# Optimization experiments

Measured on AMD Instinct MI355X. Metric: run time of the kernel, lower is better.

Reference implementation:

```python
import jax, jax.numpy as jnp
import numpy as np

EPS = 1e-05


def _nearest_upsample(x, H, W):
    # torch F.interpolate default mode='nearest': src_idx = floor(dst_idx * in/out)
    h, w = x.shape[-2], x.shape[-1]
    rows = (jnp.arange(H) * h) // H
    cols = (jnp.arange(W) * w) // W
    return x[..., rows[:, None], cols[None, :]]


def _dilate(mask, k):
    # Grayscale dilation with a flat (all-ones) k x k structuring element ==
    # k x k max filter (kornia dilation w/ ones kernel). Geodesic border: pad -inf
    p = (k - 1) // 2
    return jax.lax.reduce_window(
        mask, -jnp.inf, jax.lax.max,
        window_dimensions=(1, 1, k, k),
        window_strides=(1, 1, 1, 1),
        padding=[(0, 0), (0, 0), (p, k - 1 - p), (p, k - 1 - p)],
    )


def setup_inputs() -> dict:
    key = jax.random.key(0)
    k1, k2 = jax.random.split(key)
    small = jax.random.normal(k1, (2, 4, 1, 270, 480), dtype=jnp.float32)
    large = jax.random.uniform(k2, (2, 4, 1, 1080, 1920), dtype=jnp.float32)
    return {"small": small, "large": large, "dilate_width": 7, "sigmoid": 1}


def reference(small, large, dilate_width, sigmoid):
    B, T = small.shape[0], small.shape[1]
    s = small.reshape((B * T,) + small.shape[2:])   # [BT, C, h, w]
    l = large.reshape((B * T,) + large.shape[2:])   # [BT, C, H, W]
    H, W = l.shape[-2], l.shape[-1]
    up = _nearest_upsample(s, H, W)
    t = jax.nn.sigmoid(up) if sigmoid else up
    trans = ((t > EPS) & (t < 1.0 - EPS)).astype(l.dtype)
    if dilate_width >= 1:
        trans = _dilate(trans, dilate_width)
    out = trans * l + (1.0 - trans) * up
    return out.reshape(large.shape)
```

## Files before the change

kernel.cpp:

```cpp
#include <hip/hip_runtime.h>
#include <cmath>

#define HS 270
#define WS 480
#define HL 1080
#define WL 1920

typedef float f4 __attribute__((ext_vector_type(4)));

__global__ __launch_bounds__(256) void PRM_77824807403842_kernel(
    const float* __restrict__ sml,
    const float* __restrict__ lrg,
    const int* __restrict__ sigp,
    float* __restrict__ out)
{
    const int n = blockIdx.x * 256 + threadIdx.x;
    if (n >= HS * WS) return;
    const int bt = blockIdx.z;
    const int q = n / WS;
    const int P = n - q * WS;

    const size_t lbase = ((size_t)bt * HL + 4 * (size_t)q) * WL + 4 * (size_t)P;
    const f4* lp = reinterpret_cast<const f4*>(lrg + lbase);
    const f4 l0 = __builtin_nontemporal_load(lp + 0 * (WL / 4));
    const f4 l1 = __builtin_nontemporal_load(lp + 1 * (WL / 4));
    const f4 l2 = __builtin_nontemporal_load(lp + 2 * (WL / 4));
    const f4 l3 = __builtin_nontemporal_load(lp + 3 * (WL / 4));

    const float* sb = sml + (size_t)bt * (HS * WS);
    const int qm = q > 0 ? q - 1 : 0;
    const int qp = q < HS - 1 ? q + 1 : q;
    const int Pm = P > 0 ? P - 1 : 0;
    const int Pp = P < WS - 1 ? P + 1 : P;
    const unsigned vqm = q > 0, vqp = q < HS - 1;
    const unsigned vPm = P > 0, vPp = P < WS - 1;

    const float x00 = sb[(size_t)qm * WS + Pm], x01 = sb[(size_t)qm * WS + P], x02 = sb[(size_t)qm * WS + Pp];
    const float x10 = sb[(size_t)q  * WS + Pm], x11 = sb[(size_t)q  * WS + P], x12 = sb[(size_t)q  * WS + Pp];
    const float x20 = sb[(size_t)qp * WS + Pm], x21 = sb[(size_t)qp * WS + P], x22 = sb[(size_t)qp * WS + Pp];

    const int sig = *sigp;
    auto msk = [&](float x) -> unsigned {
        return sig ? (unsigned)((x > -11.5129154f) & (x < 11.5129054f))
                   : (unsigned)((x > 1e-5f) & (x < 0.99999f));
    };

    const unsigned M00 = msk(x00) & vqm & vPm, M01 = msk(x01) & vqm, M02 = msk(x02) & vqm & vPp;
    const unsigned M10 = msk(x10) & vPm,       M11 = msk(x11),       M12 = msk(x12) & vPp;
    const unsigned M20 = msk(x20) & vqp & vPm, M21 = msk(x21) & vqp, M22 = msk(x22) & vqp & vPp;

    const unsigned r0c0 = M00 | M10, r0c1 = M01 | M11, r0c2 = M02 | M12;
    const unsigned r2c0 = M10 | M20, r2c1 = M11 | M21, r2c2 = M12 | M22;
    const unsigned r1c0 = r0c0 | M20, r1c1 = r0c1 | M21, r1c2 = r0c2 | M22;

    const float up = x11;
    auto sel4 = [&](unsigned c0, unsigned c1, unsigned c2, f4 l) -> f4 {
        const unsigned L = c0 | c1, A = L | c2, R = c1 | c2;
        f4 o;
        o.x = L ? l.x : up;
        o.y = A ? l.y : up;
        o.z = A ? l.z : up;
        o.w = R ? l.w : up;
        return o;
    };

    f4* op = reinterpret_cast<f4*>(out + lbase);
    __builtin_nontemporal_store(sel4(r0c0, r0c1, r0c2, l0), op + 0 * (WL / 4));
    __builtin_nontemporal_store(sel4(r1c0, r1c1, r1c2, l1), op + 1 * (WL / 4));
    __builtin_nontemporal_store(sel4(r1c0, r1c1, r1c2, l2), op + 2 * (WL / 4));
    __builtin_nontemporal_store(sel4(r2c0, r2c1, r2c2, l3), op + 3 * (WL / 4));
}

extern "C" void kernel_launch(void* const* d_in, const int* in_sizes, int n_in,
                              void* d_out, int out_size, void* d_ws, size_t ws_size,
                              hipStream_t stream) {
    const float* sml = (const float*)d_in[0];
    const float* lrg = (const float*)d_in[1];
    const int* sigp = (const int*)d_in[3];
    float* outp = (float*)d_out;

    const int BT = in_sizes[1] / (HL * WL);

    dim3 grid((HS * WS + 255) / 256, 1, BT);
    dim3 block(256);
    hipLaunchKernelGGL(PRM_77824807403842_kernel, grid, block, 0, stream,
                       sml, lrg, sigp, outp);
}
```

Measured before the change: 27.00 us.

## Map one thread per large-image float4 instead of per small pixel

Each thread now handles a single float4 of one large-image row instead of a 4x4 block spanning four rows. This gives fully coalesced row-contiguous loads and stores across the wavefront and four times more threads. The nontemporal load and store hints are dropped in favour of ordinary accesses. In exchange, each thread still gathers its nine small-image neighbours, so small-image reads become redundant across the four threads sharing a small pixel, though those should mostly hit in cache.

```diff
diff --git a/kernel.cpp b/kernel.cpp
--- a/kernel.cpp
+++ b/kernel.cpp
@@ -5,6 +5,7 @@
 #define WS 480
 #define HL 1080
 #define WL 1920
+#define W4 (WL / 4)
 
 typedef float f4 __attribute__((ext_vector_type(4)));
 
@@ -14,30 +15,31 @@
     const int* __restrict__ sigp,
     float* __restrict__ out)
 {
-    const int n = blockIdx.x * 256 + threadIdx.x;
-    if (n >= HS * WS) return;
+    const int n2 = blockIdx.x * 256 + threadIdx.x;
     const int bt = blockIdx.z;
-    const int q = n / WS;
-    const int P = n - q * WS;
+    const int i = n2 / W4;
+    const int p = n2 - i * W4;
+    const int q = i >> 2;
+    const int s = i & 3;
 
-    const size_t lbase = ((size_t)bt * HL + 4 * (size_t)q) * WL + 4 * (size_t)P;
-    const f4* lp = reinterpret_cast<const f4*>(lrg + lbase);
-    const f4 l0 = __builtin_nontemporal_load(lp + 0 * (WL / 4));
-    const f4 l1 = __builtin_nontemporal_load(lp + 1 * (WL / 4));
-    const f4 l2 = __builtin_nontemporal_load(lp + 2 * (WL / 4));
-    const f4 l3 = __builtin_nontemporal_load(lp + 3 * (WL / 4));
+    const size_t lofs = ((size_t)bt * HL + i) * WL + 4 * (size_t)p;
+    const f4 lv = *reinterpret_cast<const f4*>(lrg + lofs);
 
     const float* sb = sml + (size_t)bt * (HS * WS);
-    const int qm = q > 0 ? q - 1 : 0;
-    const int qp = q < HS - 1 ? q + 1 : q;
-    const int Pm = P > 0 ? P - 1 : 0;
-    const int Pp = P < WS - 1 ? P + 1 : P;
-    const unsigned vqm = q > 0, vqp = q < HS - 1;
-    const unsigned vPm = P > 0, vPp = P < WS - 1;
+    const int rm = q > 0 ? q - 1 : 0;
+    const int rp = q < HS - 1 ? q + 1 : q;
+    const int cm = p > 0 ? p - 1 : 0;
+    const int cp = p < WS - 1 ? p + 1 : p;
+    const unsigned inc_t = (unsigned)((s < 3) & (q > 0));
+    const unsigned inc_b = (unsigned)((s > 0) & (q < HS - 1));
+    const unsigned vl = p > 0, vr = p < WS - 1;
 
-    const float x00 = sb[(size_t)qm * WS + Pm], x01 = sb[(size_t)qm * WS + P], x02 = sb[(size_t)qm * WS + Pp];
-    const float x10 = sb[(size_t)q  * WS + Pm], x11 = sb[(size_t)q  * WS + P], x12 = sb[(size_t)q  * WS + Pp];
-    const float x20 = sb[(size_t)qp * WS + Pm], x21 = sb[(size_t)qp * WS + P], x22 = sb[(size_t)qp * WS + Pp];
+    const float* r0 = sb + (size_t)rm * WS;
+    const float* r1 = sb + (size_t)q * WS;
+    const float* r2 = sb + (size_t)rp * WS;
+    const float a0 = r0[cm], a1 = r0[p], a2 = r0[cp];
+    const float b0 = r1[cm], b1 = r1[p], b2 = r1[cp];
+    const float c0 = r2[cm], c1 = r2[p], c2 = r2[cp];
 
     const int sig = *sigp;
     auto msk = [&](float x) -> unsigned {
@@ -45,30 +47,18 @@
                    : (unsigned)((x > 1e-5f) & (x < 0.99999f));
     };
 
-    const unsigned M00 = msk(x00) & vqm & vPm, M01 = msk(x01) & vqm, M02 = msk(x02) & vqm & vPp;
-    const unsigned M10 = msk(x10) & vPm,       M11 = msk(x11),       M12 = msk(x12) & vPp;
-    const unsigned M20 = msk(x20) & vqp & vPm, M21 = msk(x21) & vqp, M22 = msk(x22) & vqp & vPp;
+    const unsigned Ml = ((inc_t & msk(a0)) | msk(b0) | (inc_b & msk(c0))) & vl;
+    const unsigned Mm =  (inc_t & msk(a1)) | msk(b1) | (inc_b & msk(c1));
+    const unsigned Mr = ((inc_t & msk(a2)) | msk(b2) | (inc_b & msk(c2))) & vr;
 
-    const unsigned r0c0 = M00 | M10, r0c1 = M01 | M11, r0c2 = M02 | M12;
-    const unsigned r2c0 = M10 | M20, r2c1 = M11 | M21, r2c2 = M12 | M22;
-    const unsigned r1c0 = r0c0 | M20, r1c1 = r0c1 | M21, r1c2 = r0c2 | M22;
-
-    const float up = x11;
-    auto sel4 = [&](unsigned c0, unsigned c1, unsigned c2, f4 l) -> f4 {
-        const unsigned L = c0 | c1, A = L | c2, R = c1 | c2;
-        f4 o;
-        o.x = L ? l.x : up;
-        o.y = A ? l.y : up;
-        o.z = A ? l.z : up;
-        o.w = R ? l.w : up;
-        return o;
-    };
-
-    f4* op = reinterpret_cast<f4*>(out + lbase);
-    __builtin_nontemporal_store(sel4(r0c0, r0c1, r0c2, l0), op + 0 * (WL / 4));
-    __builtin_nontemporal_store(sel4(r1c0, r1c1, r1c2, l1), op + 1 * (WL / 4));
-    __builtin_nontemporal_store(sel4(r1c0, r1c1, r1c2, l2), op + 2 * (WL / 4));
-    __builtin_nontemporal_store(sel4(r2c0, r2c1, r2c2, l3), op + 3 * (WL / 4));
+    const float up = b1;
+    const unsigned L = Ml | Mm, A = L | Mr, R = Mm | Mr;
+    f4 o;
+    o.x = L ? lv.x : up;
+    o.y = A ? lv.y : up;
+    o.z = A ? lv.z : up;
+    o.w = R ? lv.w : up;
+    *reinterpret_cast<f4*>(out + lofs) = o;
 }
 
 extern "C" void kernel_launch(void* const* d_in, const int* in_sizes, int n_in,
@@ -81,7 +71,7 @@
 
     const int BT = in_sizes[1] / (HL * WL);
 
-    dim3 grid((HS * WS + 255) / 256, 1, BT);
+    dim3 grid(HL * W4 / 256, 1, BT);
     dim3 block(256);
     hipLaunchKernelGGL(PRM_77824807403842_kernel, grid, block, 0, stream,
                        sml, lrg, sigp, outp);
```

Measured after the change: 28.56 us. 1.06x slower.

## Split into bulk copy of large plus sparse fixup writes of upsampled values

Applied to the files above, without the earlier changes.

Replaces the single fused kernel with two launches. The first copies the large tensor into the output with plain vector loads and stores. The second reads only the small tensor, skips threads whose dilated mask covers all sixteen output pixels, and writes the upsampled value as scalar stores only where the mask is zero. This spends an extra launch and an extra pass over output addresses in exchange for less conditional selection. Because the small input is normal-distributed and the sigmoid is applied, most pixels are transitional, so the fixup kernel mostly exits early. The full copy still moves the same number of bytes.

```diff
diff --git a/kernel.cpp b/kernel.cpp
--- a/kernel.cpp
+++ b/kernel.cpp
@@ -5,12 +5,20 @@
 #define WS 480
 #define HL 1080
 #define WL 1920
+#define W4 (WL / 4)
 
 typedef float f4 __attribute__((ext_vector_type(4)));
 
-__global__ __launch_bounds__(256) void PRM_77824807403842_kernel(
+__global__ __launch_bounds__(256) void PRM_copy_kernel(
+    const float* __restrict__ lrg, float* __restrict__ out)
+{
+    const size_t idx = (size_t)(blockIdx.x * 256 + threadIdx.x) * 4;
+    const f4 v = *reinterpret_cast<const f4*>(lrg + idx);
+    *reinterpret_cast<f4*>(out + idx) = v;
+}
+
+__global__ __launch_bounds__(256) void PRM_fixup_kernel(
     const float* __restrict__ sml,
-    const float* __restrict__ lrg,
     const int* __restrict__ sigp,
     float* __restrict__ out)
 {
@@ -19,13 +27,6 @@
     const int bt = blockIdx.z;
     const int q = n / WS;
     const int P = n - q * WS;
-
-    const size_t lbase = ((size_t)bt * HL + 4 * (size_t)q) * WL + 4 * (size_t)P;
-    const f4* lp = reinterpret_cast<const f4*>(lrg + lbase);
-    const f4 l0 = __builtin_nontemporal_load(lp + 0 * (WL / 4));
-    const f4 l1 = __builtin_nontemporal_load(lp + 1 * (WL / 4));
-    const f4 l2 = __builtin_nontemporal_load(lp + 2 * (WL / 4));
-    const f4 l3 = __builtin_nontemporal_load(lp + 3 * (WL / 4));
 
     const float* sb = sml + (size_t)bt * (HS * WS);
     const int qm = q > 0 ? q - 1 : 0;
@@ -53,22 +54,22 @@
     const unsigned r2c0 = M10 | M20, r2c1 = M11 | M21, r2c2 = M12 | M22;
     const unsigned r1c0 = r0c0 | M20, r1c1 = r0c1 | M21, r1c2 = r0c2 | M22;
 
+    if (r0c0 & r0c1 & r0c2 & r2c0 & r2c1 & r2c2) return;
+
     const float up = x11;
-    auto sel4 = [&](unsigned c0, unsigned c1, unsigned c2, f4 l) -> f4 {
+    const size_t lbase = ((size_t)bt * HL + 4 * (size_t)q) * WL + 4 * (size_t)P;
+
+#pragma unroll
+    for (int s = 0; s < 4; ++s) {
+        const unsigned c0 = (s == 0) ? r0c0 : (s == 3) ? r2c0 : r1c0;
+        const unsigned c1 = (s == 0) ? r0c1 : (s == 3) ? r2c1 : r1c1;
+        const unsigned c2 = (s == 0) ? r0c2 : (s == 3) ? r2c2 : r1c2;
         const unsigned L = c0 | c1, A = L | c2, R = c1 | c2;
-        f4 o;
-        o.x = L ? l.x : up;
-        o.y = A ? l.y : up;
-        o.z = A ? l.z : up;
-        o.w = R ? l.w : up;
-        return o;
-    };
-
-    f4* op = reinterpret_cast<f4*>(out + lbase);
-    __builtin_nontemporal_store(sel4(r0c0, r0c1, r0c2, l0), op + 0 * (WL / 4));
-    __builtin_nontemporal_store(sel4(r1c0, r1c1, r1c2, l1), op + 1 * (WL / 4));
-    __builtin_nontemporal_store(sel4(r1c0, r1c1, r1c2, l2), op + 2 * (WL / 4));
-    __builtin_nontemporal_store(sel4(r2c0, r2c1, r2c2, l3), op + 3 * (WL / 4));
+        float* orow = out + lbase + (size_t)s * WL;
+        if (!L) orow[0] = up;
+        if (!A) { orow[1] = up; orow[2] = up; }
+        if (!R) orow[3] = up;
+    }
 }
 
 extern "C" void kernel_launch(void* const* d_in, const int* in_sizes, int n_in,
@@ -81,8 +82,10 @@
 
     const int BT = in_sizes[1] / (HL * WL);
 
-    dim3 grid((HS * WS + 255) / 256, 1, BT);
-    dim3 block(256);
-    hipLaunchKernelGGL(PRM_77824807403842_kernel, grid, block, 0, stream,
-                       sml, lrg, sigp, outp);
+    dim3 cgrid(BT * HL * W4 / 256, 1, 1);
+    hipLaunchKernelGGL(PRM_copy_kernel, cgrid, dim3(256), 0, stream, lrg, outp);
+
+    dim3 fgrid((HS * WS + 255) / 256, 1, BT);
+    hipLaunchKernelGGL(PRM_fixup_kernel, fgrid, dim3(256), 0, stream,
+                       sml, sigp, outp);
 }
```

After: 28.51 us. +5.6%, slower.
